# Kernel tuning notes

Measured on AMD Instinct MI355X. Metric: run time of the kernel, lower is better.

## Reference

```python
import jax, jax.numpy as jnp
import numpy as np

N = 20000      # nodes
E = 320000     # edges
H = 256        # hidden_dim
BD = 64        # bond embedding dim
MSG_IN = 2 * H + BD  # 576


def setup_inputs() -> dict:
    key = jax.random.key(0)
    ks = jax.random.split(key, 24)
    s = 0.05
    inp = {}
    inp["x"] = jax.random.randint(ks[0], (N, 3), 0, 7).astype(jnp.float32)
    inp["edge_index"] = jax.random.randint(ks[1], (2, E), 0, N).astype(jnp.int32)
    inp["edge_attr"] = jax.random.randint(ks[2], (E, 1), 0, 5).astype(jnp.float32)
    inp["batch"] = jnp.zeros((N,), jnp.int32)
    # embedding tables
    inp["atom_table"] = jax.random.normal(ks[3], (11, 64), jnp.float32) * s
    inp["charge_table"] = jax.random.normal(ks[4], (7, 32), jnp.float32) * s
    inp["hybrid_table"] = jax.random.normal(ks[5], (8, 32), jnp.float32) * s
    inp["bond_table"] = jax.random.normal(ks[6], (5, BD), jnp.float32) * s
    # 3 stacked ChemicalGraphConv layers (weights stored [in, out])
    inp["gnn_w1"] = jax.random.normal(ks[7], (3, MSG_IN, H), jnp.float32) * s
    inp["gnn_b1"] = jnp.zeros((3, H), jnp.float32)
    inp["gnn_w2"] = jax.random.normal(ks[8], (3, H, H), jnp.float32) * s
    inp["gnn_b2"] = jnp.zeros((3, H), jnp.float32)
    inp["att_w"] = jax.random.normal(ks[9], (3, BD, 1), jnp.float32) * s
    inp["att_b"] = jnp.zeros((3, 1), jnp.float32)
    # chemical_properties MLP
    inp["prop_w1"] = jax.random.normal(ks[10], (H, 128), jnp.float32) * s
    inp["prop_b1"] = jnp.zeros((128,), jnp.float32)
    inp["prop_w2"] = jax.random.normal(ks[11], (128, 32), jnp.float32) * s
    inp["prop_b2"] = jnp.zeros((32,), jnp.float32)
    # 4 functional-group pattern encoders, stacked [4, H, 16]
    inp["fg_w"] = jax.random.normal(ks[12], (4, H, 16), jnp.float32) * s
    inp["fg_b"] = jnp.zeros((4, 16), jnp.float32)
    return inp


def reference(x, edge_index, edge_attr, batch,
              atom_table, charge_table, hybrid_table, bond_table,
              gnn_w1, gnn_b1, gnn_w2, gnn_b2, att_w, att_b,
              prop_w1, prop_b1, prop_w2, prop_b2, fg_w, fg_b):
    n = x.shape[0]
    atom_types = jnp.clip(x[:, 0].astype(jnp.int32), 0, 10)
    formal_charges = jnp.clip(x[:, 2].astype(jnp.int32) + 3, 0, 6)
    hybridization = jnp.clip(x[:, 1].astype(jnp.int32), 0, 7)
    bond_types = jnp.clip(edge_attr[:, 0].astype(jnp.int32), 0, 4)
    bond_emb = bond_table[bond_types]  # [E, 64]

    h = jnp.concatenate([atom_table[atom_types],
                         charge_table[formal_charges],
                         hybrid_table[hybridization]], axis=-1)  # [N, 128]
    h = jnp.pad(h, ((0, 0), (0, H - h.shape[1])))  # pad to hidden_dim

    row, col = edge_index[0], edge_index[1]
    for l in range(3):  # 3 ChemicalGraphConv layers
        gate = jax.nn.sigmoid(bond_emb @ att_w[l] + att_b[l])            # [E, 1]
        msg = jnp.concatenate([h[row], h[col], bond_emb], axis=-1)      # [E, 576]
        msg = jax.nn.relu(msg @ gnn_w1[l] + gnn_b1[l]) @ gnn_w2[l] + gnn_b2[l]
        msg = msg * gate                                                 # [E, H]
        h = h + jax.ops.segment_sum(msg, row, num_segments=n)

    chemical_props = jax.nn.relu(h @ prop_w1 + prop_b1) @ prop_w2 + prop_b2  # [N, 32]

    # FunctionalGroupDetector: mean(encoder(h)) == mean(h) @ W + b (linear)
    pooled = jnp.mean(h, axis=0)                                   # [H]
    fg = (jnp.einsum('d,kdo->ko', pooled, fg_w) + fg_b).reshape(-1)  # [64]
    fg_features = jnp.broadcast_to(fg, (n, 64))

    return h, chemical_props, fg_features, atom_types
```

## Files before the change

### kernel.cpp

```cpp
#include <hip/hip_runtime.h>
#include <stdint.h>

typedef unsigned short u16;
typedef unsigned int   u32;
typedef unsigned long long u64;
typedef __attribute__((ext_vector_type(8))) short bf16x8;
typedef __attribute__((ext_vector_type(4))) float f32x4;

#define NN 20000
#define NE 320000
#define HD 256
#define BD 64

#define WS_PRE   0u
#define WS_W1T   20480000u
#define WS_W2I   21266432u
#define WS_PW1   21659648u
#define WS_PW2   21725184u
#define WS_PREB  21733376u
#define WS_GATE  21748736u
#define WS_POOL  21748800u
#define WS_FGV   21749824u
#define WS_CNT   21750080u
#define WS_META  21830080u

__device__ __forceinline__ u16 f2bf(float f){
  u32 u = __float_as_uint(f);
  u += 0x7fffu + ((u >> 16) & 1u);
  return (u16)(u >> 16);
}
__device__ __forceinline__ u32 pk2(float a, float b){
  return (u32)f2bf(a) | ((u32)f2bf(b) << 16);
}
__device__ __forceinline__ float bf2f(u16 u){
  return __uint_as_float((u32)u << 16);
}
__device__ __forceinline__ u32 pk2t(float a, float b){
  return __builtin_amdgcn_perm(__float_as_uint(a), __float_as_uint(b), 0x03020706u);
}
__device__ __forceinline__ u32 relu_pack(u32 a, u32 b, float p0, float p1){
  float a0 = __uint_as_float(a << 16);
  float a1 = __uint_as_float(a & 0xffff0000u);
  float b0 = __uint_as_float(b << 16);
  float b1 = __uint_as_float(b & 0xffff0000u);
  float s0 = fmaxf(a0 + b0 + p0, 0.f);
  float s1 = fmaxf(a1 + b1 + p1, 0.f);
  return pk2t(s0, s1);
}
__device__ __forceinline__ void gl_lds16(const u16* g, u16* l){
  __builtin_amdgcn_global_load_lds(
      (const __attribute__((address_space(1))) unsigned int*)g,
      (__attribute__((address_space(3))) unsigned int*)l, 16, 0, 0);
}

__global__ void setup_k(const float* __restrict__ gw1,
                        const float* __restrict__ gw2,
                        const float* __restrict__ pw1,
                        const float* __restrict__ pw2,
                        const float* __restrict__ bond_table,
                        const float* __restrict__ gb1,
                        const float* __restrict__ att_w,
                        const float* __restrict__ att_b,
                        const float* __restrict__ x,
                        const float* __restrict__ atom_table,
                        const float* __restrict__ charge_table,
                        const float* __restrict__ hybrid_table,
                        u16* __restrict__ w1t, u16* __restrict__ w2img,
                        u16* __restrict__ pw1bf, u16* __restrict__ pw2bf,
                        float* __restrict__ preb,
                        float* __restrict__ gate_tab, float* __restrict__ pooled,
                        int* __restrict__ cnt,
                        float* __restrict__ h0, float* __restrict__ out_at){
  int i = blockIdx.x*256 + threadIdx.x;
  if (i < 442368){
    float v = gw1[i];
    int l = i / 147456;
    int r = i - l*147456;
    int srow = r >> 8, c = r & 255;
    if (srow < 512){
      int dc = (srow < 256) ? c : (256 + c);
      w1t[((size_t)l*512 + dc)*256 + (srow & 255)] = f2bf(v);
    }
  } else if (i < 638976){
    int t = i - 442368;
    float v = gw2[t];
    int l = t >> 16;
    int rest = t & 65535;
    int k = rest >> 8, c = rest & 255;
    int ks = k >> 5, k5 = k & 31;
    int kc = k5 >> 3, j = k5 & 7;
    int s = kc ^ ((c >> 1) & 3);
    w2img[(((l*8 + ks)*256 + c)*4 + s)*8 + j] = f2bf(v);
  } else if (i < 671744){
    int t = i - 638976;
    float v = pw1[t];
    int k = t >> 7, o = t & 127;
    pw1bf[o*256 + k] = f2bf(v);
  } else if (i < 675840){
    int t = i - 671744;
    float v = pw2[t];
    int k = t >> 5, o = t & 31;
    pw2bf[o*128 + k] = f2bf(v);
  } else if (i < 679680){
    int t = i - 675840;
    int l = t / 1280;
    int r = t - l*1280;
    int bt = r >> 8, c = r & 255;
    float s = gb1[l*HD + c];
    for (int d = 0; d < BD; ++d)
      s += bond_table[bt*BD + d] * gw1[(l*576 + 512 + d)*256 + c];
    preb[(l*5 + bt)*256 + c] = s;
  } else if (i < 679695){
    int t = i - 679680;
    int l = t / 5, b = t - 5*l;
    float s = att_b[l];
    for (int d = 0; d < BD; ++d) s += bond_table[b*BD + d] * att_w[l*BD + d];
    gate_tab[t] = 1.0f / (1.0f + __expf(-s));
  } else if (i < 679951){
    pooled[i - 679695] = 0.0f;
  } else if (i < 699951){
    cnt[i - 679951] = 0;
  } else if (i < 1339951){
    int t = i - 699951;
    int n = t >> 5, sub = t & 31, c0 = sub*8;
    int at = (int)x[n*3 + 0]; at = at < 0 ? 0 : (at > 10 ? 10 : at);
    float4 v0 = {0.f,0.f,0.f,0.f}, v1 = {0.f,0.f,0.f,0.f};
    if (c0 < 64){
      v0 = *(const float4*)(atom_table + at*64 + c0);
      v1 = *(const float4*)(atom_table + at*64 + c0 + 4);
    } else if (c0 < 96){
      int fc = (int)x[n*3 + 2] + 3; fc = fc < 0 ? 0 : (fc > 6 ? 6 : fc);
      v0 = *(const float4*)(charge_table + fc*32 + (c0 - 64));
      v1 = *(const float4*)(charge_table + fc*32 + (c0 - 64) + 4);
    } else if (c0 < 128){
      int hy = (int)x[n*3 + 1]; hy = hy < 0 ? 0 : (hy > 7 ? 7 : hy);
      v0 = *(const float4*)(hybrid_table + hy*32 + (c0 - 96));
      v1 = *(const float4*)(hybrid_table + hy*32 + (c0 - 96) + 4);
    }
    *(float4*)(h0 + (size_t)n*HD + c0)     = v0;
    *(float4*)(h0 + (size_t)n*HD + c0 + 4) = v1;
    if (sub == 0) out_at[n] = (float)at;
  }
}

__global__ void hist_k(const int* __restrict__ eidx, int* __restrict__ cnt){
  int e = blockIdx.x*256 + threadIdx.x;
  int r = eidx[e]; r = r < 0 ? 0 : (r >= NN ? NN-1 : r);
  atomicAdd(&cnt[r], 1);
}

__launch_bounds__(1024)
__global__ void scan_k(int* __restrict__ cnt){
  __shared__ int part[1024];
  int t = threadIdx.x;
  int base = t*20;
  int loc[20];
  int s = 0;
  #pragma unroll
  for (int j = 0; j < 20; ++j){
    int idx = base + j;
    int v = (idx < NN) ? cnt[idx] : 0;
    loc[j] = v; s += v;
  }
  part[t] = s; __syncthreads();
  for (int off = 1; off < 1024; off <<= 1){
    int v = (t >= off) ? part[t-off] : 0;
    __syncthreads();
    part[t] += v;
    __syncthreads();
  }
  int run = part[t] - s;
  #pragma unroll
  for (int j = 0; j < 20; ++j){
    int idx = base + j;
    if (idx < NN){ cnt[idx] = run; run += loc[j]; }
  }
}

__global__ void scatter_k(const int* __restrict__ eidx,
                          const float* __restrict__ eattr,
                          int* __restrict__ cur,
                          int2* __restrict__ smeta){
  int e = blockIdx.x*256 + threadIdx.x;
  int r = eidx[e];        r = r < 0 ? 0 : (r >= NN ? NN-1 : r);
  int c = eidx[NE + e];   c = c < 0 ? 0 : (c >= NN ? NN-1 : c);
  int bt = (int)eattr[e]; bt = bt < 0 ? 0 : (bt > 4 ? 4 : bt);
  int pos = atomicAdd(&cur[r], 1);
  if (pos >= 0 && pos < NE){
    int2 m; m.x = r | (bt << 20); m.y = c;
    smeta[pos] = m;
  }
}

__launch_bounds__(256, 2)
__global__ void pre_k(const float* __restrict__ h,
                      const u16* __restrict__ w1t,
                      u16* __restrict__ pre, int layer){
  __shared__ u16 a_lds[64*40];
  __shared__ u16 b_lds[512*40];
  const int tid = threadIdx.x;
  const int n0 = blockIdx.x * 64;
  const int w = tid >> 6, lane = tid & 63, g = lane >> 4, lr = lane & 15;
  const int rstage = tid >> 2, q = tid & 3;
  int arow = n0 + rstage; if (arow >= NN) arow = NN-1;
  const float* hrow = h + (size_t)arow*HD;
  const u16* bp0 = w1t + ((size_t)layer*512 + tid)*256;
  const u16* bp1 = bp0 + 256*256;

  f32x4 acc[4][8];
  for (int mi = 0; mi < 4; ++mi)
    #pragma unroll
    for (int nj = 0; nj < 8; ++nj)
      acc[mi][nj] = (f32x4){0.f,0.f,0.f,0.f};

  for (int ks = 0; ks < 8; ++ks){
    __syncthreads();
    {
      const float* src = hrow + ks*32 + q*8;
      float4 f0 = *(const float4*)src;
      float4 f1 = *(const float4*)(src + 4);
      uint4 av;
      av.x = pk2(f0.x,f0.y); av.y = pk2(f0.z,f0.w);
      av.z = pk2(f1.x,f1.y); av.w = pk2(f1.z,f1.w);
      *(uint4*)(a_lds + rstage*40 + q*8) = av;
    }
    {
      const u16* s0p = bp0 + ks*32;
      const u16* s1p = bp1 + ks*32;
      uint4 s0 = *(const uint4*)(s0p);
      uint4 s1 = *(const uint4*)(s0p + 8);
      uint4 s2 = *(const uint4*)(s0p + 16);
      uint4 s3 = *(const uint4*)(s0p + 24);
      u16* dst = b_lds + tid*40;
      *(uint4*)(dst)      = s0;
      *(uint4*)(dst + 8)  = s1;
      *(uint4*)(dst + 16) = s2;
      *(uint4*)(dst + 24) = s3;
      uint4 t0 = *(const uint4*)(s1p);
      uint4 t1 = *(const uint4*)(s1p + 8);
      uint4 t2v = *(const uint4*)(s1p + 16);
      uint4 t3 = *(const uint4*)(s1p + 24);
      u16* dst1 = b_lds + (tid + 256)*40;
      *(uint4*)(dst1)      = t0;
      *(uint4*)(dst1 + 8)  = t1;
      *(uint4*)(dst1 + 16) = t2v;
      *(uint4*)(dst1 + 24) = t3;
    }
    __syncthreads();
    bf16x8 af[4], bfr[8];
    for (int mi = 0; mi < 4; ++mi)
      af[mi] = *(const bf16x8*)(a_lds + (mi*16 + lr)*40 + g*8);
    #pragma unroll
    for (int nj = 0; nj < 8; ++nj)
      bfr[nj] = *(const bf16x8*)(b_lds + (w*128 + nj*16 + lr)*40 + g*8);
    for (int mi = 0; mi < 4; ++mi)
      #pragma unroll
      for (int nj = 0; nj < 8; ++nj)
        acc[mi][nj] = __builtin_amdgcn_mfma_f32_16x16x32_bf16(af[mi], bfr[nj], acc[mi][nj], 0, 0, 0);
  }

  for (int mi = 0; mi < 4; ++mi)
    #pragma unroll
    for (int nj = 0; nj < 8; ++nj)
      for (int p = 0; p < 4; ++p){
        int re = mi*16 + g*4 + p;
        int n = n0 + re;
        int col = w*128 + nj*16 + lr;
        if (n < NN)
          pre[(size_t)n*512 + col] = f2bf(acc[mi][nj][p]);
      }
}

__launch_bounds__(512, 4)
__global__ void edge_msg_k(const int2* __restrict__ smeta,
                           const u16* __restrict__ pre,
                           const float* __restrict__ prebg,
                           const u16* __restrict__ w2img,
                           const float* __restrict__ b2g,
                           const float* __restrict__ gate_tab,
                           float* __restrict__ h,
                           int layer){
  __shared__ u16 b_lds[16384];
  __shared__ u16 t_lds[64*264];
  __shared__ int   row_l[64];
  __shared__ float gate_l[64];
  __shared__ float gps_l[64];
  __shared__ u64   mask_l;

  const int tid = threadIdx.x;
  const int bid = blockIdx.x;
  const int blk = (bid & 7)*625 + (bid >> 3);
  const int eBase = blk * 64;
  const int w = tid >> 6, lane = tid & 63, g = lane >> 4, lr = lane & 15;
  const int rstage = tid >> 3, q = tid & 7;

  const size_t wbase = (size_t)layer*65536;

  #pragma unroll
  for (int b = 0; b < 2; ++b)
    #pragma unroll
    for (int j = 0; j < 2; ++j)
      gl_lds16(w2img + wbase + (size_t)(b*256 + w*32 + j*16)*32 + lane*8,
               b_lds + b*8192 + w*1024 + j*512);

  int2 m0 = smeta[eBase + rstage];
  const int rI  = m0.x & 0xFFFFF;
  const int btI = (m0.x >> 20) & 7;
  const int cI  = m0.y;

  if (tid < 64){
    int2 mm = smeta[eBase + tid];
    int r = mm.x & 0xFFFFF;
    row_l[tid] = r;
    float gt = gate_tab[layer*5 + ((mm.x >> 20) & 7)];
    gate_l[tid] = gt;
    float ps = gt;
    #pragma unroll
    for (int off = 1; off < 64; off <<= 1){
      float o = __shfl_up(ps, off);
      if (tid >= off) ps += o;
    }
    gps_l[tid] = ps;
    int rprev = __shfl_up(r, 1);
    bool fl = (tid > 0) && (r != rprev);
    u64 mk = __ballot(fl);
    if (tid == 0) mask_l = mk;
  }

  {
    const u16* p1 = pre + (size_t)rI*512;
    const u16* p2 = pre + (size_t)cI*512 + 256;
    const float* pb = prebg + (size_t)(layer*5 + btI)*256;
    uint4 v1[4], v2[4];
    #pragma unroll
    for (int it = 0; it < 4; ++it){
      int c0 = it*64 + q*8;
      v1[it] = *(const uint4*)(p1 + c0);
      v2[it] = *(const uint4*)(p2 + c0);
    }
    #pragma unroll
    for (int it = 0; it < 4; ++it){
      int c0 = it*64 + q*8;
      float4 pa = *(const float4*)(pb + c0);
      float4 pc = *(const float4*)(pb + c0 + 4);
      uint4 ov;
      ov.x = relu_pack(v1[it].x, v2[it].x, pa.x, pa.y);
      ov.y = relu_pack(v1[it].y, v2[it].y, pa.z, pa.w);
      ov.z = relu_pack(v1[it].z, v2[it].z, pc.x, pc.y);
      ov.w = relu_pack(v1[it].w, v2[it].w, pc.z, pc.w);
      *(uint4*)(t_lds + rstage*264 + c0) = ov;
    }
  }

  __syncthreads();

  f32x4 acc[4][2];
  for (int mi = 0; mi < 4; ++mi)
    for (int nj = 0; nj < 2; ++nj)
      acc[mi][nj] = (f32x4){0.f,0.f,0.f,0.f};

  const int sw = (g ^ ((lr >> 1) & 3)) << 3;

  #pragma unroll
  for (int ks = 0; ks < 8; ++ks){
    if (ks >= 1 && ks < 7){
      #pragma unroll
      for (int j = 0; j < 2; ++j)
        gl_lds16(w2img + wbase + (size_t)((ks+1)*256 + w*32 + j*16)*32 + lane*8,
                 b_lds + ((ks+1)&1)*8192 + w*1024 + j*512);
      asm volatile("s_waitcnt vmcnt(2)" ::: "memory");
    } else if (ks == 0){
      asm volatile("s_waitcnt vmcnt(2)" ::: "memory");
    } else {
      asm volatile("s_waitcnt vmcnt(0)" ::: "memory");
    }
    const u16* bb = b_lds + (ks&1)*8192 + w*1024;
    bf16x8 af[4], bfr[2];
    for (int nj = 0; nj < 2; ++nj)
      bfr[nj] = *(const bf16x8*)(bb + (nj*16 + lr)*32 + sw);
    for (int mi = 0; mi < 4; ++mi)
      af[mi] = *(const bf16x8*)(t_lds + (mi*16 + lr)*264 + ks*32 + g*8);
    __builtin_amdgcn_s_setprio(1);
    for (int mi = 0; mi < 4; ++mi)
      for (int nj = 0; nj < 2; ++nj)
        acc[mi][nj] = __builtin_amdgcn_mfma_f32_16x16x32_bf16(af[mi], bfr[nj], acc[mi][nj], 0, 0, 0);
    __builtin_amdgcn_s_setprio(0);
  }

  {
    for (int mi = 0; mi < 4; ++mi)
      for (int nj = 0; nj < 2; ++nj){
        u16* mb = b_lds + nj*8192 + w*1024 + lr*64;
        float v[4];
        #pragma unroll
        for (int p = 0; p < 4; ++p){
          int re = mi*16 + g*4 + p;
          v[p] = acc[mi][nj][p] * gate_l[re];
        }
        int slot = (mi*2 + (g >> 1)) ^ (lr & 7);
        uint2 pkv; pkv.x = pk2t(v[0], v[1]); pkv.y = pk2t(v[2], v[3]);
        *(uint2*)(mb + slot*8 + (g & 1)*4) = pkv;
      }
  }
  __syncthreads();

  {
    const int cl = tid & 255, half = tid >> 8;
    float b2v = b2g[layer*HD + cl];
    u64 mk = mask_l;
    u32 m32 = (u32)(mk >> (half ? 32 : 0));
    m32 = __builtin_amdgcn_readfirstlane(m32);
    const u16* mb = b_lds + ((cl >> 4) & 1)*8192 + (cl >> 5)*1024 + (cl & 15)*64;
    float run = 0.f;
    float gprev = half ? gps_l[31] : 0.f;
    #pragma unroll
    for (int e8l = 0; e8l < 4; ++e8l){
      int e8 = half*4 + e8l;
      bf16x8 mv = *(const bf16x8*)(mb + ((e8 ^ (cl & 7)) << 3));
      #pragma unroll
      for (int j = 0; j < 8; ++j){
        int el = e8l*8 + j;
        run += bf2f((u16)mv[j]);
        bool fl = (el == 31) || ((m32 >> (el + 1)) & 1u);
        if (fl){
          int ae = half*32 + el;
          float gc = gps_l[ae];
          int rr = row_l[ae];
          atomicAdd(h + (size_t)rr*HD + cl, fmaf(b2v, gc - gprev, run));
          gprev = gc;
          run = 0.f;
        }
      }
    }
  }
}

__global__ void pool_k(const float* __restrict__ h,
                       float* __restrict__ pooled){
  int c = threadIdx.x;
  int r0 = blockIdx.x * 50;
  float s = 0.f;
  for (int r = r0; r < r0 + 50; ++r)
    s += h[(size_t)r*HD + c];
  atomicAdd(&pooled[c], s);
}

__global__ void fg_k(const float* __restrict__ pooled,
                     const float* __restrict__ fg_w,
                     const float* __restrict__ fg_b,
                     float* __restrict__ fg_vals){
  int o = threadIdx.x;
  int k = o >> 4, j = o & 15;
  float s = 0.f;
  for (int d = 0; d < HD; ++d) s += pooled[d] * fg_w[(size_t)k*HD*16 + d*16 + j];
  fg_vals[o] = s / (float)NN + fg_b[k*16 + j];
}

__global__ void bcast_fg_k(const float* __restrict__ fg_vals,
                           float* __restrict__ out_fg){
  __shared__ float fv[64];
  if (threadIdx.x < 64) fv[threadIdx.x] = fg_vals[threadIdx.x];
  __syncthreads();
  int i = blockIdx.x*256 + threadIdx.x;
  out_fg[i] = fv[i & 63];
}

__launch_bounds__(256, 3)
__global__ void props_mfma_k(const float* __restrict__ h,
                             const u16* __restrict__ pw1bf,
                             const float* __restrict__ pb1,
                             const u16* __restrict__ pw2bf,
                             const float* __restrict__ pb2,
                             float* __restrict__ outp){
  __shared__ u16 a_lds[64*40];
  __shared__ u16 b2_lds[128*40];
  __shared__ u16 t2[64*136];
  const int tid = threadIdx.x;
  const int n0 = blockIdx.x*64;
  const int w = tid >> 6, lane = tid & 63, g = lane >> 4, lr = lane & 15;
  const int rstage = tid >> 2, q = tid & 3;
  int arow = n0 + rstage; if (arow >= NN) arow = NN-1;
  const float* hrow = h + (size_t)arow*HD;

  const int colb = tid >> 1, halfb = tid & 1;

  f32x4 acc[4][2];
  for (int mi = 0; mi < 4; ++mi)
    for (int nj = 0; nj < 2; ++nj)
      acc[mi][nj] = (f32x4){0.f,0.f,0.f,0.f};

  for (int ks = 0; ks < 8; ++ks){
    __syncthreads();
    {
      const float* src = hrow + ks*32 + q*8;
      float4 f0 = *(const float4*)src;
      float4 f1 = *(const float4*)(src + 4);
      uint4 av;
      av.x = pk2(f0.x,f0.y); av.y = pk2(f0.z,f0.w);
      av.z = pk2(f1.x,f1.y); av.w = pk2(f1.z,f1.w);
      *(uint4*)(a_lds + rstage*40 + q*8) = av;
    }
    {
      const u16* src = pw1bf + colb*256 + ks*32 + halfb*16;
      uint4 s0 = *(const uint4*)src;
      uint4 s1 = *(const uint4*)(src + 8);
      u16* dst = b2_lds + colb*40 + halfb*16;
      *(uint4*)dst = s0; *(uint4*)(dst + 8) = s1;
    }
    __syncthreads();
    bf16x8 af[4], bfr[2];
    for (int mi = 0; mi < 4; ++mi)
      af[mi] = *(const bf16x8*)(a_lds + (mi*16 + lr)*40 + g*8);
    for (int nj = 0; nj < 2; ++nj)
      bfr[nj] = *(const bf16x8*)(b2_lds + (w*32 + nj*16 + lr)*40 + g*8);
    for (int mi = 0; mi < 4; ++mi)
      for (int nj = 0; nj < 2; ++nj)
        acc[mi][nj] = __builtin_amdgcn_mfma_f32_16x16x32_bf16(af[mi], bfr[nj], acc[mi][nj], 0, 0, 0);
  }

  {
    float b1v[2];
    for (int nj = 0; nj < 2; ++nj) b1v[nj] = pb1[w*32 + nj*16 + lr];
    for (int mi = 0; mi < 4; ++mi)
      for (int nj = 0; nj < 2; ++nj){
        int colt = w*32 + nj*16 + lr;
        for (int p = 0; p < 4; ++p){
          float v = acc[mi][nj][p] + b1v[nj];
          v = v > 0.f ? v : 0.f;
          t2[(mi*16 + g*4 + p)*136 + colt] = f2bf(v);
        }
      }
  }
  __syncthreads();

  {
    int col = tid >> 3, part = tid & 7;
    const u16* src = pw2bf + col*128 + part*16;
    u16* dst = b2_lds + col*136 + part*16;
    *(uint4*)dst       = *(const uint4*)src;
    *(uint4*)(dst + 8) = *(const uint4*)(src + 8);
  }
  __syncthreads();

  {
    f32x4 acc2[2];
    for (int nj = 0; nj < 2; ++nj) acc2[nj] = (f32x4){0.f,0.f,0.f,0.f};
    for (int ks = 0; ks < 4; ++ks){
      bf16x8 af = *(const bf16x8*)(t2 + (w*16 + lr)*136 + ks*32 + g*8);
      for (int nj = 0; nj < 2; ++nj){
        bf16x8 bf = *(const bf16x8*)(b2_lds + (nj*16 + lr)*136 + ks*32 + g*8);
        acc2[nj] = __builtin_amdgcn_mfma_f32_16x16x32_bf16(af, bf, acc2[nj], 0, 0, 0);
      }
    }
    for (int nj = 0; nj < 2; ++nj)
      for (int p = 0; p < 4; ++p){
        int n = n0 + w*16 + g*4 + p;
        int col = nj*16 + lr;
        if (n < NN)
          outp[(size_t)n*32 + col] = acc2[nj][p] + pb2[col];
      }
  }
}

extern "C" void kernel_launch(void* const* d_in, const int* in_sizes, int n_in,
                              void* d_out, int out_size, void* d_ws, size_t ws_size,
                              hipStream_t stream) {
  const float* x            = (const float*)d_in[0];
  const int*   eidx         = (const int*)  d_in[1];
  const float* eattr        = (const float*)d_in[2];
  const float* atom_table   = (const float*)d_in[4];
  const float* charge_table = (const float*)d_in[5];
  const float* hybrid_table = (const float*)d_in[6];
  const float* bond_table   = (const float*)d_in[7];
  const float* gw1          = (const float*)d_in[8];
  const float* gb1          = (const float*)d_in[9];
  const float* gw2          = (const float*)d_in[10];
  const float* gb2          = (const float*)d_in[11];
  const float* attw         = (const float*)d_in[12];
  const float* attb         = (const float*)d_in[13];
  const float* pw1          = (const float*)d_in[14];
  const float* pb1          = (const float*)d_in[15];
  const float* pw2          = (const float*)d_in[16];
  const float* pb2          = (const float*)d_in[17];
  const float* fgw          = (const float*)d_in[18];
  const float* fgb          = (const float*)d_in[19];

  float* out       = (float*)d_out;
  float* out_h     = out;
  float* out_props = out + (size_t)NN*HD;
  float* out_fg    = out_props + (size_t)NN*32;
  float* out_at    = out_fg + (size_t)NN*64;

  char* ws = (char*)d_ws;
  u16*   pre      = (u16*)  (ws + WS_PRE);
  u16*   w1t      = (u16*)  (ws + WS_W1T);
  u16*   w2img    = (u16*)  (ws + WS_W2I);
  u16*   pw1bf    = (u16*)  (ws + WS_PW1);
  u16*   pw2bf    = (u16*)  (ws + WS_PW2);
  float* prebg    = (float*)(ws + WS_PREB);
  float* gate_tab = (float*)(ws + WS_GATE);
  float* pooled   = (float*)(ws + WS_POOL);
  float* fg_vals  = (float*)(ws + WS_FGV);
  int*   cnt      = (int*)  (ws + WS_CNT);
  int2*  smeta    = (int2*) (ws + WS_META);

  setup_k<<<5235, 256, 0, stream>>>(gw1, gw2, pw1, pw2, bond_table, gb1, attw, attb,
                                    x, atom_table, charge_table, hybrid_table,
                                    w1t, w2img, pw1bf, pw2bf, prebg, gate_tab, pooled,
                                    cnt, out_h, out_at);

  hist_k<<<1250, 256, 0, stream>>>(eidx, cnt);
  scan_k<<<1, 1024, 0, stream>>>(cnt);
  scatter_k<<<1250, 256, 0, stream>>>(eidx, eattr, cnt, smeta);

  for (int l = 0; l < 3; ++l){
    pre_k<<<313, 256, 0, stream>>>(out_h, w1t, pre, l);
    edge_msg_k<<<5000, 512, 0, stream>>>(smeta, pre, prebg, w2img,
                                         gb2, gate_tab, out_h, l);
  }

  pool_k<<<400, 256, 0, stream>>>(out_h, pooled);
  fg_k<<<1, 64, 0, stream>>>(pooled, fgw, fgb, fg_vals);
  props_mfma_k<<<313, 256, 0, stream>>>(out_h, pw1bf, pb1, pw2bf, pb2, out_props);
  bcast_fg_k<<<5000, 256, 0, stream>>>(fg_vals, out_fg);
}
```

Measured before the change: 392.1 us.

## Load W2 fragments directly into registers and drop B LDS buffer for occupancy

The second-layer weight matrix is now stored plainly transposed, and each wave loads its MFMA B fragments straight from global memory (L2-resident) into registers, double-buffered, instead of staging them through a 32KB LDS buffer with async global-to-LDS loads. The epilogue reuses the activation tile LDS for the message reduction after a new barrier. Launch bounds go from 4 to 6 blocks per CU to use the freed LDS. The aim is to cut LDS footprint and so raise occupancy on this latency-bound edge kernel. The cost is more global/L2 traffic per wave, B-load latency exposed in registers, and added register pressure under the tighter bound.

```diff
diff --git a/kernel.cpp b/kernel.cpp
--- a/kernel.cpp
+++ b/kernel.cpp
@@ -14,7 +14,7 @@
 
 #define WS_PRE   0u
 #define WS_W1T   20480000u
-#define WS_W2I   21266432u
+#define WS_W2T   21266432u
 #define WS_PW1   21659648u
 #define WS_PW2   21725184u
 #define WS_PREB  21733376u
@@ -46,11 +46,6 @@
   float s0 = fmaxf(a0 + b0 + p0, 0.f);
   float s1 = fmaxf(a1 + b1 + p1, 0.f);
   return pk2t(s0, s1);
-}
-__device__ __forceinline__ void gl_lds16(const u16* g, u16* l){
-  __builtin_amdgcn_global_load_lds(
-      (const __attribute__((address_space(1))) unsigned int*)g,
-      (__attribute__((address_space(3))) unsigned int*)l, 16, 0, 0);
 }
 
 __global__ void setup_k(const float* __restrict__ gw1,
@@ -65,7 +60,7 @@
                         const float* __restrict__ atom_table,
                         const float* __restrict__ charge_table,
                         const float* __restrict__ hybrid_table,
-                        u16* __restrict__ w1t, u16* __restrict__ w2img,
+                        u16* __restrict__ w1t, u16* __restrict__ w2t,
                         u16* __restrict__ pw1bf, u16* __restrict__ pw2bf,
                         float* __restrict__ preb,
                         float* __restrict__ gate_tab, float* __restrict__ pooled,
@@ -85,12 +80,9 @@
     int t = i - 442368;
     float v = gw2[t];
     int l = t >> 16;
-    int rest = t & 65535;
-    int k = rest >> 8, c = rest & 255;
-    int ks = k >> 5, k5 = k & 31;
-    int kc = k5 >> 3, j = k5 & 7;
-    int s = kc ^ ((c >> 1) & 3);
-    w2img[(((l*8 + ks)*256 + c)*4 + s)*8 + j] = f2bf(v);
+    int k = (t >> 8) & 255;
+    int c = t & 255;
+    w2t[(((size_t)l*256 + c) << 8) | k] = f2bf(v);
   } else if (i < 671744){
     int t = i - 638976;
     float v = pw1[t];
@@ -271,16 +263,15 @@
       }
 }
 
-__launch_bounds__(512, 4)
+__launch_bounds__(512, 6)
 __global__ void edge_msg_k(const int2* __restrict__ smeta,
                            const u16* __restrict__ pre,
                            const float* __restrict__ prebg,
-                           const u16* __restrict__ w2img,
+                           const u16* __restrict__ w2t,
                            const float* __restrict__ b2g,
                            const float* __restrict__ gate_tab,
                            float* __restrict__ h,
                            int layer){
-  __shared__ u16 b_lds[16384];
   __shared__ u16 t_lds[64*264];
   __shared__ int   row_l[64];
   __shared__ float gate_l[64];
@@ -294,14 +285,10 @@
   const int w = tid >> 6, lane = tid & 63, g = lane >> 4, lr = lane & 15;
   const int rstage = tid >> 3, q = tid & 7;
 
-  const size_t wbase = (size_t)layer*65536;
-
-  #pragma unroll
-  for (int b = 0; b < 2; ++b)
-    #pragma unroll
-    for (int j = 0; j < 2; ++j)
-      gl_lds16(w2img + wbase + (size_t)(b*256 + w*32 + j*16)*32 + lane*8,
-               b_lds + b*8192 + w*1024 + j*512);
+  const u16* w2p = w2t + (((size_t)layer*256 + w*32 + lr) << 8) + g*8;
+
+  bf16x8 bA0 = *(const bf16x8*)(w2p);
+  bf16x8 bA1 = *(const bf16x8*)(w2p + 4096);
 
   int2 m0 = smeta[eBase + rstage];
   const int rI  = m0.x & 0xFFFFF;
@@ -359,38 +346,41 @@
     for (int nj = 0; nj < 2; ++nj)
       acc[mi][nj] = (f32x4){0.f,0.f,0.f,0.f};
 
-  const int sw = (g ^ ((lr >> 1) & 3)) << 3;
-
-  #pragma unroll
-  for (int ks = 0; ks < 8; ++ks){
-    if (ks >= 1 && ks < 7){
-      #pragma unroll
-      for (int j = 0; j < 2; ++j)
-        gl_lds16(w2img + wbase + (size_t)((ks+1)*256 + w*32 + j*16)*32 + lane*8,
-                 b_lds + ((ks+1)&1)*8192 + w*1024 + j*512);
-      asm volatile("s_waitcnt vmcnt(2)" ::: "memory");
-    } else if (ks == 0){
-      asm volatile("s_waitcnt vmcnt(2)" ::: "memory");
-    } else {
-      asm volatile("s_waitcnt vmcnt(0)" ::: "memory");
-    }
-    const u16* bb = b_lds + (ks&1)*8192 + w*1024;
-    bf16x8 af[4], bfr[2];
-    for (int nj = 0; nj < 2; ++nj)
-      bfr[nj] = *(const bf16x8*)(bb + (nj*16 + lr)*32 + sw);
-    for (int mi = 0; mi < 4; ++mi)
-      af[mi] = *(const bf16x8*)(t_lds + (mi*16 + lr)*264 + ks*32 + g*8);
-    __builtin_amdgcn_s_setprio(1);
-    for (int mi = 0; mi < 4; ++mi)
-      for (int nj = 0; nj < 2; ++nj)
-        acc[mi][nj] = __builtin_amdgcn_mfma_f32_16x16x32_bf16(af[mi], bfr[nj], acc[mi][nj], 0, 0, 0);
-    __builtin_amdgcn_s_setprio(0);
-  }
+  {
+    bf16x8 bB0, bB1, afv[4];
+#define LDAF(ks) { _Pragma("unroll") for (int mi = 0; mi < 4; ++mi) \
+      afv[mi] = *(const bf16x8*)(t_lds + (mi*16 + lr)*264 + (ks)*32 + g*8); }
+#define MMA(B0,B1) { __builtin_amdgcn_s_setprio(1); \
+      _Pragma("unroll") for (int mi = 0; mi < 4; ++mi){ \
+        acc[mi][0] = __builtin_amdgcn_mfma_f32_16x16x32_bf16(afv[mi], B0, acc[mi][0], 0, 0, 0); \
+        acc[mi][1] = __builtin_amdgcn_mfma_f32_16x16x32_bf16(afv[mi], B1, acc[mi][1], 0, 0, 0); } \
+      __builtin_amdgcn_s_setprio(0); }
+
+    bB0 = *(const bf16x8*)(w2p + 32);          bB1 = *(const bf16x8*)(w2p + 4096 + 32);
+    LDAF(0); MMA(bA0, bA1);
+    bA0 = *(const bf16x8*)(w2p + 64);          bA1 = *(const bf16x8*)(w2p + 4096 + 64);
+    LDAF(1); MMA(bB0, bB1);
+    bB0 = *(const bf16x8*)(w2p + 96);          bB1 = *(const bf16x8*)(w2p + 4096 + 96);
+    LDAF(2); MMA(bA0, bA1);
+    bA0 = *(const bf16x8*)(w2p + 128);         bA1 = *(const bf16x8*)(w2p + 4096 + 128);
+    LDAF(3); MMA(bB0, bB1);
+    bB0 = *(const bf16x8*)(w2p + 160);         bB1 = *(const bf16x8*)(w2p + 4096 + 160);
+    LDAF(4); MMA(bA0, bA1);
+    bA0 = *(const bf16x8*)(w2p + 192);         bA1 = *(const bf16x8*)(w2p + 4096 + 192);
+    LDAF(5); MMA(bB0, bB1);
+    bB0 = *(const bf16x8*)(w2p + 224);         bB1 = *(const bf16x8*)(w2p + 4096 + 224);
+    LDAF(6); MMA(bA0, bA1);
+    LDAF(7); MMA(bB0, bB1);
+#undef LDAF
+#undef MMA
+  }
+
+  __syncthreads();
 
   {
     for (int mi = 0; mi < 4; ++mi)
       for (int nj = 0; nj < 2; ++nj){
-        u16* mb = b_lds + nj*8192 + w*1024 + lr*64;
+        u16* mb = t_lds + nj*8192 + w*1024 + lr*64;
         float v[4];
         #pragma unroll
         for (int p = 0; p < 4; ++p){
@@ -410,7 +400,7 @@
     u64 mk = mask_l;
     u32 m32 = (u32)(mk >> (half ? 32 : 0));
     m32 = __builtin_amdgcn_readfirstlane(m32);
-    const u16* mb = b_lds + ((cl >> 4) & 1)*8192 + (cl >> 5)*1024 + (cl & 15)*64;
+    const u16* mb = t_lds + ((cl >> 4) & 1)*8192 + (cl >> 5)*1024 + (cl & 15)*64;
     float run = 0.f;
     float gprev = half ? gps_l[31] : 0.f;
     #pragma unroll
@@ -594,7 +584,7 @@
   char* ws = (char*)d_ws;
   u16*   pre      = (u16*)  (ws + WS_PRE);
   u16*   w1t      = (u16*)  (ws + WS_W1T);
-  u16*   w2img    = (u16*)  (ws + WS_W2I);
+  u16*   w2t      = (u16*)  (ws + WS_W2T);
   u16*   pw1bf    = (u16*)  (ws + WS_PW1);
   u16*   pw2bf    = (u16*)  (ws + WS_PW2);
   float* prebg    = (float*)(ws + WS_PREB);
@@ -606,7 +596,7 @@
 
   setup_k<<<5235, 256, 0, stream>>>(gw1, gw2, pw1, pw2, bond_table, gb1, attw, attb,
                                     x, atom_table, charge_table, hybrid_table,
-                                    w1t, w2img, pw1bf, pw2bf, prebg, gate_tab, pooled,
+                                    w1t, w2t, pw1bf, pw2bf, prebg, gate_tab, pooled,
                                     cnt, out_h, out_at);
 
   hist_k<<<1250, 256, 0, stream>>>(eidx, cnt);
@@ -615,7 +605,7 @@
 
   for (int l = 0; l < 3; ++l){
     pre_k<<<313, 256, 0, stream>>>(out_h, w1t, pre, l);
-    edge_msg_k<<<5000, 512, 0, stream>>>(smeta, pre, prebg, w2img,
+    edge_msg_k<<<5000, 512, 0, stream>>>(smeta, pre, prebg, w2t,
                                          gb2, gate_tab, out_h, l);
   }
 
```

Measured after the change: 478.3 us. 22.0% more time.

## Split pre_k output columns across grid y and fold bias before gating

Applied to the files above, without the earlier changes.

pre_k now launches a 2D grid so that each block computes only half of the 512 output columns. This halves the B tile in LDS and the accumulator registers, and the launch bound rises to 4 blocks per CU, which doubles the number of blocks available on the device. The A tile (h rows) is now loaded and converted twice, once per half. In edge_msg_k the b2 bias is added to the accumulator before gating, which removes the prefix-sum scan of gates and the per-segment fmaf correction. The bias is now rounded to bf16 along with the message, a small precision change.

```diff
diff --git a/kernel.cpp b/kernel.cpp
--- a/kernel.cpp
+++ b/kernel.cpp
@@ -192,25 +192,24 @@
   }
 }
 
-__launch_bounds__(256, 2)
+__launch_bounds__(256, 4)
 __global__ void pre_k(const float* __restrict__ h,
                       const u16* __restrict__ w1t,
                       u16* __restrict__ pre, int layer){
   __shared__ u16 a_lds[64*40];
-  __shared__ u16 b_lds[512*40];
+  __shared__ u16 b_lds[256*40];
   const int tid = threadIdx.x;
   const int n0 = blockIdx.x * 64;
+  const int half = blockIdx.y;
   const int w = tid >> 6, lane = tid & 63, g = lane >> 4, lr = lane & 15;
   const int rstage = tid >> 2, q = tid & 3;
   int arow = n0 + rstage; if (arow >= NN) arow = NN-1;
   const float* hrow = h + (size_t)arow*HD;
-  const u16* bp0 = w1t + ((size_t)layer*512 + tid)*256;
-  const u16* bp1 = bp0 + 256*256;
-
-  f32x4 acc[4][8];
+  const u16* bp = w1t + ((size_t)layer*512 + (size_t)half*256 + tid)*256;
+
+  f32x4 acc[4][4];
   for (int mi = 0; mi < 4; ++mi)
-    #pragma unroll
-    for (int nj = 0; nj < 8; ++nj)
+    for (int nj = 0; nj < 4; ++nj)
       acc[mi][nj] = (f32x4){0.f,0.f,0.f,0.f};
 
   for (int ks = 0; ks < 8; ++ks){
@@ -225,49 +224,35 @@
       *(uint4*)(a_lds + rstage*40 + q*8) = av;
     }
     {
-      const u16* s0p = bp0 + ks*32;
-      const u16* s1p = bp1 + ks*32;
-      uint4 s0 = *(const uint4*)(s0p);
-      uint4 s1 = *(const uint4*)(s0p + 8);
-      uint4 s2 = *(const uint4*)(s0p + 16);
-      uint4 s3 = *(const uint4*)(s0p + 24);
+      const u16* src = bp + ks*32;
+      uint4 s0 = *(const uint4*)(src);
+      uint4 s1 = *(const uint4*)(src + 8);
+      uint4 s2 = *(const uint4*)(src + 16);
+      uint4 s3 = *(const uint4*)(src + 24);
       u16* dst = b_lds + tid*40;
       *(uint4*)(dst)      = s0;
       *(uint4*)(dst + 8)  = s1;
       *(uint4*)(dst + 16) = s2;
       *(uint4*)(dst + 24) = s3;
-      uint4 t0 = *(const uint4*)(s1p);
-      uint4 t1 = *(const uint4*)(s1p + 8);
-      uint4 t2v = *(const uint4*)(s1p + 16);
-      uint4 t3 = *(const uint4*)(s1p + 24);
-      u16* dst1 = b_lds + (tid + 256)*40;
-      *(uint4*)(dst1)      = t0;
-      *(uint4*)(dst1 + 8)  = t1;
-      *(uint4*)(dst1 + 16) = t2v;
-      *(uint4*)(dst1 + 24) = t3;
     }
     __syncthreads();
-    bf16x8 af[4], bfr[8];
+    bf16x8 af[4], bfr[4];
     for (int mi = 0; mi < 4; ++mi)
       af[mi] = *(const bf16x8*)(a_lds + (mi*16 + lr)*40 + g*8);
-    #pragma unroll
-    for (int nj = 0; nj < 8; ++nj)
-      bfr[nj] = *(const bf16x8*)(b_lds + (w*128 + nj*16 + lr)*40 + g*8);
-    for (int mi = 0; mi < 4; ++mi)
-      #pragma unroll
-      for (int nj = 0; nj < 8; ++nj)
+    for (int nj = 0; nj < 4; ++nj)
+      bfr[nj] = *(const bf16x8*)(b_lds + (w*64 + nj*16 + lr)*40 + g*8);
+    for (int mi = 0; mi < 4; ++mi)
+      for (int nj = 0; nj < 4; ++nj)
         acc[mi][nj] = __builtin_amdgcn_mfma_f32_16x16x32_bf16(af[mi], bfr[nj], acc[mi][nj], 0, 0, 0);
   }
 
   for (int mi = 0; mi < 4; ++mi)
-    #pragma unroll
-    for (int nj = 0; nj < 8; ++nj)
+    for (int nj = 0; nj < 4; ++nj)
       for (int p = 0; p < 4; ++p){
         int re = mi*16 + g*4 + p;
         int n = n0 + re;
-        int col = w*128 + nj*16 + lr;
         if (n < NN)
-          pre[(size_t)n*512 + col] = f2bf(acc[mi][nj][p]);
+          pre[(size_t)n*512 + half*256 + w*64 + nj*16 + lr] = f2bf(acc[mi][nj][p]);
       }
 }
 
@@ -284,7 +269,6 @@
   __shared__ u16 t_lds[64*264];
   __shared__ int   row_l[64];
   __shared__ float gate_l[64];
-  __shared__ float gps_l[64];
   __shared__ u64   mask_l;
 
   const int tid = threadIdx.x;
@@ -312,15 +296,7 @@
     int2 mm = smeta[eBase + tid];
     int r = mm.x & 0xFFFFF;
     row_l[tid] = r;
-    float gt = gate_tab[layer*5 + ((mm.x >> 20) & 7)];
-    gate_l[tid] = gt;
-    float ps = gt;
-    #pragma unroll
-    for (int off = 1; off < 64; off <<= 1){
-      float o = __shfl_up(ps, off);
-      if (tid >= off) ps += o;
-    }
-    gps_l[tid] = ps;
+    gate_l[tid] = gate_tab[layer*5 + ((mm.x >> 20) & 7)];
     int rprev = __shfl_up(r, 1);
     bool fl = (tid > 0) && (r != rprev);
     u64 mk = __ballot(fl);
@@ -388,6 +364,8 @@
   }
 
   {
+    float b2v[2];
+    for (int nj = 0; nj < 2; ++nj) b2v[nj] = b2g[layer*HD + w*32 + nj*16 + lr];
     for (int mi = 0; mi < 4; ++mi)
       for (int nj = 0; nj < 2; ++nj){
         u16* mb = b_lds + nj*8192 + w*1024 + lr*64;
@@ -395,7 +373,7 @@
         #pragma unroll
         for (int p = 0; p < 4; ++p){
           int re = mi*16 + g*4 + p;
-          v[p] = acc[mi][nj][p] * gate_l[re];
+          v[p] = (acc[mi][nj][p] + b2v[nj]) * gate_l[re];
         }
         int slot = (mi*2 + (g >> 1)) ^ (lr & 7);
         uint2 pkv; pkv.x = pk2t(v[0], v[1]); pkv.y = pk2t(v[2], v[3]);
@@ -406,13 +384,11 @@
 
   {
     const int cl = tid & 255, half = tid >> 8;
-    float b2v = b2g[layer*HD + cl];
     u64 mk = mask_l;
     u32 m32 = (u32)(mk >> (half ? 32 : 0));
     m32 = __builtin_amdgcn_readfirstlane(m32);
     const u16* mb = b_lds + ((cl >> 4) & 1)*8192 + (cl >> 5)*1024 + (cl & 15)*64;
     float run = 0.f;
-    float gprev = half ? gps_l[31] : 0.f;
     #pragma unroll
     for (int e8l = 0; e8l < 4; ++e8l){
       int e8 = half*4 + e8l;
@@ -423,11 +399,8 @@
         run += bf2f((u16)mv[j]);
         bool fl = (el == 31) || ((m32 >> (el + 1)) & 1u);
         if (fl){
-          int ae = half*32 + el;
-          float gc = gps_l[ae];
-          int rr = row_l[ae];
-          atomicAdd(h + (size_t)rr*HD + cl, fmaf(b2v, gc - gprev, run));
-          gprev = gc;
+          int rr = row_l[half*32 + el];
+          atomicAdd(h + (size_t)rr*HD + cl, run);
           run = 0.f;
         }
       }
@@ -614,7 +587,7 @@
   scatter_k<<<1250, 256, 0, stream>>>(eidx, eattr, cnt, smeta);
 
   for (int l = 0; l < 3; ++l){
-    pre_k<<<313, 256, 0, stream>>>(out_h, w1t, pre, l);
+    pre_k<<<dim3(313, 2), 256, 0, stream>>>(out_h, w1t, pre, l);
     edge_msg_k<<<5000, 512, 0, stream>>>(smeta, pre, prebg, w2img,
                                          gb2, gate_tab, out_h, l);
   }
```

After: 377.9 us, median of 2. 1.04x faster.
